# Optimization experiments

Measured on AMD Instinct MI355X. Metric: run time of the kernel, lower is better.

Reference implementation:

```python
import jax, jax.numpy as jnp
import numpy as np

B, NB, K, S = 4, 131072, 32, 768


def setup_inputs() -> dict:
    key = jax.random.key(0)
    k1, k2, k3, k4 = jax.random.split(key, 4)
    N = B * NB
    logits_embedding = jax.random.normal(k1, (N, 4), dtype=jnp.float32)
    logits_seediness = jax.random.normal(k2, (N, 1), dtype=jnp.float32)
    coords = jax.random.uniform(k3, (N, 3), dtype=jnp.float32, minval=0.0, maxval=float(S))
    inst = jax.random.randint(k4, (N,), 0, K).astype(jnp.float32)
    batch = jnp.repeat(jnp.arange(B, dtype=jnp.float32), NB)
    labels = jnp.concatenate(
        [batch[:, None], coords, jnp.zeros((N, 1), jnp.float32), inst[:, None]], axis=1)
    return {"logits_embedding": logits_embedding,
            "logits_seediness": logits_seediness,
            "labels": labels}


def reference(logits_embedding, logits_seediness, labels):
    half = S / 2.0
    # coords_embedding = emb[:, :3] + (voxel_coords - S/2) / (S/2)
    ce = logits_embedding[:, :3] + (labels[:, 1:4] - half) / half          # [N,3]
    sigma = logits_embedding[:, 3]                                          # [N]
    seed = logits_seediness.reshape(-1)                                     # [N]
    inst = labels[:, 5].astype(jnp.int32)                                   # [N]

    # batch ids are contiguous by construction -> reshape to [B, NB, ...]
    ce = ce.reshape(B, NB, 3)
    sigma = sigma.reshape(B, NB)
    seed = seed.reshape(B, NB)
    inst = inst.reshape(B, NB)

    onehot = (inst[:, :, None] == jnp.arange(K)[None, None, :]).astype(jnp.float32)  # [B,NB,K]
    counts = jnp.maximum(onehot.sum(axis=1), 1.0)                                    # [B,K]

    centers = jnp.einsum('bnk,bnd->bkd', onehot, ce) / counts[:, :, None]            # [B,K,3]
    sigmas = jnp.einsum('bnk,bn->bk', onehot, sigma) / counts                        # [B,K]

    # squared distance of every point to every instance center
    diff = ce[:, :, None, :] - centers[:, None, :, :]                                # [B,NB,K,3]
    dist2 = jnp.sum(diff * diff, axis=-1)                                            # [B,NB,K]

    arg = jnp.clip(dist2 / (2.0 * sigmas[:, None, :] ** 2), 1e-7, 100.0)
    p = jnp.exp(-arg)                                                                # [B,NB,K]

    # mask loss: log(p) == -arg exactly
    mask_loss = -(onehot * (-arg) + (1.0 - onehot) * jnp.log1p(-p)).sum(axis=(1, 2)) / NB / K  # [B]

    smooth = (onehot * jnp.abs(sigma[:, :, None] - sigmas[:, None, :])).sum(axis=1) / counts
    smooth_loss = smooth.sum(axis=1) / K                                             # [B]

    seed_term = (onehot * (seed[:, :, None] - p) ** 2).sum(axis=1) / counts
    seed_loss = seed_term.sum(axis=1) / K                                            # [B]

    # inter-cluster hinge, sum over unordered pairs i<j, denom K*(K-1)
    cdiff = centers[:, :, None, :] - centers[:, None, :, :]                          # [B,K,K,3]
    cd2 = jnp.sum(cdiff * cdiff, axis=-1)
    eye = jnp.eye(K, dtype=jnp.float32)[None]
    d = jnp.sqrt(jnp.where(eye > 0, 1.0, cd2))                                       # safe sqrt on diag
    hinge = jnp.maximum(0.0, 2.0 * 0.5 - d) ** 2 * (1.0 - eye)
    inter_loss = hinge.sum(axis=(1, 2)) / 2.0 / (K * (K - 1))                        # [B]

    loss = jnp.mean(mask_loss + smooth_loss + inter_loss + seed_loss)

    # accuracy: assign each point to nearest center (instance ids are 0..K-1)
    pred = jnp.argmin(dist2, axis=2)                                                 # [B,NB]
    acc = jnp.mean((pred == inst).astype(jnp.float32))
    return loss, jax.lax.stop_gradient(acc)
```

## Files before the change

### kernel.cpp

```cpp
#include <hip/hip_runtime.h>

#define B_ 4
#define NB_ 131072
#define K_ 32
#define N_ (B_*NB_)
#define BK_ (B_*K_)
#define NACC 256
#define ABLK 64
#define PTS_PER_ACC 2048

#define ACC_OFF  0
#define FIN_OFF  (NACC*5*K_)
#define PART_OFF (FIN_OFF + 6*BK_)

__global__ __launch_bounds__(1024) void k_accum(
    const float4* __restrict__ emb, const float* __restrict__ labels,
    float* __restrict__ ws)
{
    __shared__ float sacc[5*K_];
    int tid = threadIdx.x;
    if (tid < 5*K_) sacc[tid] = 0.f;
    __syncthreads();
    int start = blockIdx.x * PTS_PER_ACC;
    #pragma unroll
    for (int i = 0; i < PTS_PER_ACC/1024; ++i) {
        int n = start + i*1024 + tid;
        float4 e = emb[n];
        const float* lr = labels + (size_t)n*6;
        float c1 = lr[1];
        float2 c23 = *reinterpret_cast<const float2*>(lr + 2);
        int inst = ((int)lr[5]) & 31;
        float cex = e.x + (c1    - 384.f)/384.f;
        float cey = e.y + (c23.x - 384.f)/384.f;
        float cez = e.z + (c23.y - 384.f)/384.f;
        atomicAdd(&sacc[0*K_+inst], cex);
        atomicAdd(&sacc[1*K_+inst], cey);
        atomicAdd(&sacc[2*K_+inst], cez);
        atomicAdd(&sacc[3*K_+inst], e.w);
        atomicAdd(&sacc[4*K_+inst], 1.0f);
    }
    __syncthreads();
    if (tid < 5*K_) ws[ACC_OFF + blockIdx.x*5*K_ + tid] = sacc[tid];
}

__global__ __launch_bounds__(256) void k_main(
    const float4* __restrict__ emb, const float* __restrict__ seedp,
    const float* __restrict__ labels, float* __restrict__ ws,
    float4* __restrict__ part)
{
    __shared__ float s_raw[5*K_];
    __shared__ float s_fin[6*K_];
    int tid = threadIdx.x;
    int n = blockIdx.x * 256 + tid;
    int b = blockIdx.x >> 9;

    if (tid < 5*K_) {
        float a = 0.f;
        const float* base = ws + ACC_OFF + (size_t)b*ABLK*5*K_ + tid;
        #pragma unroll 8
        for (int j = 0; j < ABLK; ++j) a += base[(size_t)j*5*K_];
        s_raw[tid] = a;
    }
    __syncthreads();
    if (tid < K_) {
        float cnt = fmaxf(s_raw[4*K_+tid], 1.f);
        float inv = 1.f / cnt;
        float cx = s_raw[0*K_+tid] * inv;
        float cy = s_raw[1*K_+tid] * inv;
        float cz = s_raw[2*K_+tid] * inv;
        float sg = s_raw[3*K_+tid] * inv;
        float i2s = 1.f / (2.f*sg*sg);
        s_fin[0*K_+tid] = cx;
        s_fin[1*K_+tid] = cy;
        s_fin[2*K_+tid] = cz;
        s_fin[3*K_+tid] = sg;
        s_fin[4*K_+tid] = inv;
        s_fin[5*K_+tid] = i2s;
        if ((blockIdx.x & 511) == 0) {
            float* fin = ws + FIN_OFF;
            fin[0*BK_ + b*K_+tid] = cx;
            fin[1*BK_ + b*K_+tid] = cy;
            fin[2*BK_ + b*K_+tid] = cz;
            fin[3*BK_ + b*K_+tid] = sg;
            fin[4*BK_ + b*K_+tid] = inv;
            fin[5*BK_ + b*K_+tid] = i2s;
        }
    }
    __syncthreads();

    float4 e = emb[n];
    const float* lr = labels + (size_t)n*6;
    float c1 = lr[1];
    float2 c23 = *reinterpret_cast<const float2*>(lr + 2);
    int inst = ((int)lr[5]) & 31;
    float sd = seedp[n];
    float cex = e.x + (c1    - 384.f)/384.f;
    float cey = e.y + (c23.x - 384.f)/384.f;
    float cez = e.z + (c23.y - 384.f)/384.f;
    float sigma = e.w;

    unsigned bestpk = 0xffffffffu;
    float msum = 0.f;
    #pragma unroll
    for (int k = 0; k < K_; ++k) {
        float dx = cex - s_fin[0*K_+k];
        float dy = cey - s_fin[1*K_+k];
        float dz = cez - s_fin[2*K_+k];
        float d2 = dx*dx + dy*dy + dz*dz;
        unsigned pk = (__float_as_uint(d2) & ~31u) | (unsigned)k;
        bestpk = min(bestpk, pk);
        float arg = d2 * s_fin[5*K_+k];
        if (__any(arg < 15.f)) {
            float argc = fminf(fmaxf(arg, 1e-7f), 100.f);
            float p = __expf(-argc);
            float l1p = __logf(1.f - p);
            msum += (arg < 15.f) ? l1p : 0.f;
        }
    }
    int bi = (int)(bestpk & 31u);

    float dxI = cex - s_fin[0*K_+inst];
    float dyI = cey - s_fin[1*K_+inst];
    float dzI = cez - s_fin[2*K_+inst];
    float d2I = dxI*dxI + dyI*dyI + dzI*dzI;
    float argRawI = d2I * s_fin[5*K_+inst];
    float argI = fminf(fmaxf(argRawI, 1e-7f), 100.f);
    float pI = __expf(-argI);
    if (argRawI < 15.f) msum -= __logf(1.f - pI);
    msum -= argI;

    float inv_in = s_fin[4*K_+inst];
    float smoothv = fabsf(sigma - s_fin[3*K_+inst]) * inv_in;
    float dsd = sd - pI;
    float seedv = dsd*dsd*inv_in;
    float accv = (bi == inst) ? 1.0f : 0.0f;

    float v0 = msum, v1 = smoothv, v2 = seedv, v3 = accv;
    for (int off = 32; off; off >>= 1) {
        v0 += __shfl_down(v0, off);
        v1 += __shfl_down(v1, off);
        v2 += __shfl_down(v2, off);
        v3 += __shfl_down(v3, off);
    }
    __shared__ float sred[4][4];
    int wid = tid >> 6, lane = tid & 63;
    if (lane == 0) { sred[wid][0]=v0; sred[wid][1]=v1; sred[wid][2]=v2; sred[wid][3]=v3; }
    __syncthreads();
    if (tid == 0) {
        float r0=0.f,r1=0.f,r2=0.f,r3=0.f;
        for (int w = 0; w < 4; ++w) { r0+=sred[w][0]; r1+=sred[w][1]; r2+=sred[w][2]; r3+=sred[w][3]; }
        part[blockIdx.x] = make_float4(r0, r1, r2, r3);
    }
}

__global__ __launch_bounds__(256) void k_final(
    const float* __restrict__ ws, const float* __restrict__ part,
    float* __restrict__ out)
{
    int tid = threadIdx.x;

    int pair = tid >> 4;
    int lane16 = tid & 15;
    int f = pair >> 2, b = pair & 3;
    float v = 0.f;
    #pragma unroll
    for (int j = 0; j < 32; ++j) {
        int blk = b*512 + lane16*32 + j;
        v += part[blk*4 + f];
    }
    v += __shfl_down(v, 8);
    v += __shfl_down(v, 4);
    v += __shfl_down(v, 2);
    v += __shfl_down(v, 1);
    __shared__ float S[16];
    if (lane16 == 0) S[pair] = v;

    float h = 0.f;
    for (int idx = tid; idx < B_*K_*K_; idx += 256) {
        int bb = idx >> 10;
        int ij = idx & 1023;
        int i = ij >> 5, j = ij & 31;
        if (i != j) {
            const float* fin = ws + FIN_OFF;
            float dx = fin[0*BK_ + bb*K_+i] - fin[0*BK_ + bb*K_+j];
            float dy = fin[1*BK_ + bb*K_+i] - fin[1*BK_ + bb*K_+j];
            float dz = fin[2*BK_ + bb*K_+i] - fin[2*BK_ + bb*K_+j];
            float cd2 = dx*dx + dy*dy + dz*dz;
            float d = sqrtf(cd2);
            float hg = fmaxf(0.f, 1.0f - d);
            h += hg*hg;
        }
    }
    for (int off = 32; off; off >>= 1) h += __shfl_down(h, off);
    __shared__ float sh[4];
    int wid = tid >> 6, lane = tid & 63;
    if (lane == 0) sh[wid] = h;
    __syncthreads();

    if (tid == 0) {
        float ht = sh[0]+sh[1]+sh[2]+sh[3];
        float loss = 0.f;
        for (int bb = 0; bb < B_; ++bb) {
            float mask_l   = -S[0*4+bb] / (float)NB_ / (float)K_;
            float smooth_l =  S[1*4+bb] / (float)K_;
            float seed_l   =  S[2*4+bb] / (float)K_;
            loss += mask_l + smooth_l + seed_l;
        }
        loss = loss / (float)B_ + ht / (2.0f * (float)(K_*(K_-1)) * (float)B_);
        float acc = (S[3*4+0]+S[3*4+1]+S[3*4+2]+S[3*4+3]) / (float)N_;
        out[0] = loss;
        out[1] = acc;
    }
}

extern "C" void kernel_launch(void* const* d_in, const int* in_sizes, int n_in,
                              void* d_out, int out_size, void* d_ws, size_t ws_size,
                              hipStream_t stream)
{
    const float4* emb    = (const float4*)d_in[0];
    const float*  seedp  = (const float*)d_in[1];
    const float*  labels = (const float*)d_in[2];
    float* ws  = (float*)d_ws;
    float* out = (float*)d_out;

    k_accum <<<NACC,    1024, 0, stream>>>(emb, labels, ws);
    k_main  <<<N_/256,  256,  0, stream>>>(emb, seedp, labels, ws,
                                           (float4*)(ws + PART_OFF));
    k_final <<<1,       256,  0, stream>>>(ws, ws + PART_OFF, out);
}
```

Baseline: 42.69 us.

## Replicate shared accumulators, transpose partial layout, pack centers as float4

k_accum now keeps four copies of the shared per-instance accumulators, chosen by wavefront index, to cut LDS atomic contention. The copies are summed before being written in a transposed [feature][block] layout. That layout lets k_main reduce its 64 partials per batch with contiguous float4 loads instead of strided scalar loads. k_main packs center xyz and the inverse 2σ² term into one float4 in LDS, so each k iteration does a single wide LDS read, and it adds a launch_bounds occupancy hint. The costs are extra LDS and a final four-way sum per block.

```diff
diff --git a/kernel.cpp b/kernel.cpp
--- a/kernel.cpp
+++ b/kernel.cpp
@@ -8,18 +8,20 @@
 #define NACC 256
 #define ABLK 64
 #define PTS_PER_ACC 2048
+#define NMAIN (N_/256)
 
 #define ACC_OFF  0
-#define FIN_OFF  (NACC*5*K_)
+#define FIN_OFF  (5*K_*NACC)
 #define PART_OFF (FIN_OFF + 6*BK_)
 
 __global__ __launch_bounds__(1024) void k_accum(
     const float4* __restrict__ emb, const float* __restrict__ labels,
     float* __restrict__ ws)
 {
-    __shared__ float sacc[5*K_];
+    __shared__ float sacc[4][5*K_];
     int tid = threadIdx.x;
-    if (tid < 5*K_) sacc[tid] = 0.f;
+    int rep = (tid >> 6) & 3;
+    if (tid < 4*5*K_) ((float*)sacc)[tid] = 0.f;
     __syncthreads();
     int start = blockIdx.x * PTS_PER_ACC;
     #pragma unroll
@@ -33,33 +35,40 @@
         float cex = e.x + (c1    - 384.f)/384.f;
         float cey = e.y + (c23.x - 384.f)/384.f;
         float cez = e.z + (c23.y - 384.f)/384.f;
-        atomicAdd(&sacc[0*K_+inst], cex);
-        atomicAdd(&sacc[1*K_+inst], cey);
-        atomicAdd(&sacc[2*K_+inst], cez);
-        atomicAdd(&sacc[3*K_+inst], e.w);
-        atomicAdd(&sacc[4*K_+inst], 1.0f);
-    }
-    __syncthreads();
-    if (tid < 5*K_) ws[ACC_OFF + blockIdx.x*5*K_ + tid] = sacc[tid];
-}
-
-__global__ __launch_bounds__(256) void k_main(
+        atomicAdd(&sacc[rep][0*K_+inst], cex);
+        atomicAdd(&sacc[rep][1*K_+inst], cey);
+        atomicAdd(&sacc[rep][2*K_+inst], cez);
+        atomicAdd(&sacc[rep][3*K_+inst], e.w);
+        atomicAdd(&sacc[rep][4*K_+inst], 1.0f);
+    }
+    __syncthreads();
+    if (tid < 5*K_) {
+        float a = sacc[0][tid] + sacc[1][tid] + sacc[2][tid] + sacc[3][tid];
+        ws[ACC_OFF + tid*NACC + blockIdx.x] = a;
+    }
+}
+
+__global__ __launch_bounds__(256, 8) void k_main(
     const float4* __restrict__ emb, const float* __restrict__ seedp,
     const float* __restrict__ labels, float* __restrict__ ws,
     float4* __restrict__ part)
 {
     __shared__ float s_raw[5*K_];
-    __shared__ float s_fin[6*K_];
+    __shared__ float4 s_c4[K_];
+    __shared__ float s_sig[K_], s_inv[K_];
     int tid = threadIdx.x;
     int n = blockIdx.x * 256 + tid;
     int b = blockIdx.x >> 9;
 
     if (tid < 5*K_) {
-        float a = 0.f;
-        const float* base = ws + ACC_OFF + (size_t)b*ABLK*5*K_ + tid;
-        #pragma unroll 8
-        for (int j = 0; j < ABLK; ++j) a += base[(size_t)j*5*K_];
-        s_raw[tid] = a;
+        const float4* row = (const float4*)(ws + ACC_OFF + (size_t)tid*NACC + b*ABLK);
+        float4 a4 = make_float4(0.f,0.f,0.f,0.f);
+        #pragma unroll
+        for (int j = 0; j < ABLK/4; ++j) {
+            float4 v = row[j];
+            a4.x += v.x; a4.y += v.y; a4.z += v.z; a4.w += v.w;
+        }
+        s_raw[tid] = (a4.x + a4.y) + (a4.z + a4.w);
     }
     __syncthreads();
     if (tid < K_) {
@@ -70,12 +79,9 @@
         float cz = s_raw[2*K_+tid] * inv;
         float sg = s_raw[3*K_+tid] * inv;
         float i2s = 1.f / (2.f*sg*sg);
-        s_fin[0*K_+tid] = cx;
-        s_fin[1*K_+tid] = cy;
-        s_fin[2*K_+tid] = cz;
-        s_fin[3*K_+tid] = sg;
-        s_fin[4*K_+tid] = inv;
-        s_fin[5*K_+tid] = i2s;
+        s_c4[tid] = make_float4(cx, cy, cz, i2s);
+        s_sig[tid] = sg;
+        s_inv[tid] = inv;
         if ((blockIdx.x & 511) == 0) {
             float* fin = ws + FIN_OFF;
             fin[0*BK_ + b*K_+tid] = cx;
@@ -89,11 +95,11 @@
     __syncthreads();
 
     float4 e = emb[n];
+    float sd = seedp[n];
     const float* lr = labels + (size_t)n*6;
     float c1 = lr[1];
     float2 c23 = *reinterpret_cast<const float2*>(lr + 2);
     int inst = ((int)lr[5]) & 31;
-    float sd = seedp[n];
     float cex = e.x + (c1    - 384.f)/384.f;
     float cey = e.y + (c23.x - 384.f)/384.f;
     float cez = e.z + (c23.y - 384.f)/384.f;
@@ -103,13 +109,14 @@
     float msum = 0.f;
     #pragma unroll
     for (int k = 0; k < K_; ++k) {
-        float dx = cex - s_fin[0*K_+k];
-        float dy = cey - s_fin[1*K_+k];
-        float dz = cez - s_fin[2*K_+k];
+        float4 c = s_c4[k];
+        float dx = cex - c.x;
+        float dy = cey - c.y;
+        float dz = cez - c.z;
         float d2 = dx*dx + dy*dy + dz*dz;
         unsigned pk = (__float_as_uint(d2) & ~31u) | (unsigned)k;
         bestpk = min(bestpk, pk);
-        float arg = d2 * s_fin[5*K_+k];
+        float arg = d2 * c.w;
         if (__any(arg < 15.f)) {
             float argc = fminf(fmaxf(arg, 1e-7f), 100.f);
             float p = __expf(-argc);
@@ -119,18 +126,19 @@
     }
     int bi = (int)(bestpk & 31u);
 
-    float dxI = cex - s_fin[0*K_+inst];
-    float dyI = cey - s_fin[1*K_+inst];
-    float dzI = cez - s_fin[2*K_+inst];
+    float4 cI = s_c4[inst];
+    float dxI = cex - cI.x;
+    float dyI = cey - cI.y;
+    float dzI = cez - cI.z;
     float d2I = dxI*dxI + dyI*dyI + dzI*dzI;
-    float argRawI = d2I * s_fin[5*K_+inst];
+    float argRawI = d2I * cI.w;
     float argI = fminf(fmaxf(argRawI, 1e-7f), 100.f);
     float pI = __expf(-argI);
     if (argRawI < 15.f) msum -= __logf(1.f - pI);
     msum -= argI;
 
-    float inv_in = s_fin[4*K_+inst];
-    float smoothv = fabsf(sigma - s_fin[3*K_+inst]) * inv_in;
+    float inv_in = s_inv[inst];
+    float smoothv = fabsf(sigma - s_sig[inst]) * inv_in;
     float dsd = sd - pI;
     float seedv = dsd*dsd*inv_in;
     float accv = (bi == inst) ? 1.0f : 0.0f;
@@ -223,8 +231,8 @@
     float* ws  = (float*)d_ws;
     float* out = (float*)d_out;
 
-    k_accum <<<NACC,    1024, 0, stream>>>(emb, labels, ws);
-    k_main  <<<N_/256,  256,  0, stream>>>(emb, seedp, labels, ws,
-                                           (float4*)(ws + PART_OFF));
-    k_final <<<1,       256,  0, stream>>>(ws, ws + PART_OFF, out);
-}
+    k_accum <<<NACC,   1024, 0, stream>>>(emb, labels, ws);
+    k_main  <<<NMAIN,  256,  0, stream>>>(emb, seedp, labels, ws,
+                                          (float4*)(ws + PART_OFF));
+    k_final <<<1,      256,  0, stream>>>(ws, ws + PART_OFF, out);
+}
```

Result: slower. 46.68 us (+9.4%).
